# Optimization experiments

Hardware: AMD Instinct MI355X
Metric: run time of the kernel (lower is better)

## Reference

```python
import jax, jax.numpy as jnp
import numpy as np

N = 50000       # nodes
E_RAND = 800000 # random edges (avg degree 16); self loops appended
IN, HID, H, OUT = 256, 64, 4, 256
NEG_SLOPE = 0.2


def setup_inputs() -> dict:
    key = jax.random.key(0)
    ks = jax.random.split(key, 8)
    x = jax.random.normal(ks[0], (N, IN), dtype=jnp.float32)
    er = jax.random.randint(ks[1], (2, E_RAND), 0, N, dtype=jnp.int32)
    loops = jnp.arange(N, dtype=jnp.int32)
    edge_index = jnp.concatenate([er, jnp.stack([loops, loops])], axis=1)  # [2, E_RAND+N]
    # xavier-ish scaled params
    W1 = jax.random.normal(ks[2], (H * HID, IN), jnp.float32) * (2.0 / (IN + H * HID)) ** 0.5
    a1_src = jax.random.normal(ks[3], (H, HID), jnp.float32) * 0.1
    a1_dst = jax.random.normal(ks[4], (H, HID), jnp.float32) * 0.1
    W2 = jax.random.normal(ks[5], (OUT, H * HID), jnp.float32) * (2.0 / (H * HID + OUT)) ** 0.5
    a2_src = jax.random.normal(ks[6], (1, OUT), jnp.float32) * 0.1
    a2_dst = jax.random.normal(ks[7], (1, OUT), jnp.float32) * 0.1
    return {"x": x, "edge_index": edge_index, "W1": W1, "a1_src": a1_src,
            "a1_dst": a1_dst, "W2": W2, "a2_src": a2_src, "a2_dst": a2_dst}


def gat_layer(h, W, a_src, a_dst, src, dst, concat):
    n = h.shape[0]
    nh, nf = a_src.shape
    hp = (h @ W.T).reshape(n, nh, nf)                 # [N,H,F]
    e = (hp[src] * a_src).sum(-1) + (hp[dst] * a_dst).sum(-1)  # [E,H]
    e = jnp.where(e > 0, e, NEG_SLOPE * e)            # leaky_relu
    e_max = jax.ops.segment_max(e, dst, num_segments=n)
    ex = jnp.exp(e - e_max[dst])
    e_sum = jax.ops.segment_sum(ex, dst, num_segments=n)
    alpha = ex / (e_sum[dst] + 1e-16)                 # [E,H]
    out = jax.ops.segment_sum(hp[src] * alpha[..., None], dst, num_segments=n)
    return out.reshape(n, nh * nf) if concat else out.mean(axis=1)


def reference(x, edge_index, W1, a1_src, a1_dst, W2, a2_src, a2_dst):
    src, dst = edge_index[0], edge_index[1]
    h = jax.nn.relu(gat_layer(x, W1, a1_src, a1_dst, src, dst, True))
    return gat_layer(h, W2, a2_src, a2_dst, src, dst, False)
```

## Files before the change

kernel.cpp:

```cpp
#include <hip/hip_runtime.h>
#include <math.h>


typedef __attribute__((ext_vector_type(8))) short short8;
typedef __attribute__((ext_vector_type(4))) float f32x4;
typedef _Float16 half8 __attribute__((ext_vector_type(8)));

__device__ inline short f2bf(float f) {
    unsigned u = __float_as_uint(f);
    unsigned r = (u + 0x7FFF + ((u >> 16) & 1)) >> 16;
    return (short)r;
}
__device__ inline float bf2f(short b) {
    return __uint_as_float(((unsigned)(unsigned short)b) << 16);
}
__device__ inline unsigned short f2h(float f) {
    _Float16 h = (_Float16)f;
    unsigned short u;
    __builtin_memcpy(&u, &h, 2);
    return u;
}
__device__ inline float h2f(unsigned short u) {
    _Float16 h;
    __builtin_memcpy(&h, &u, 2);
    return (float)h;
}

__global__ void convert_w(const float* __restrict__ W, short* __restrict__ Whi,
                          short* __restrict__ Wlo, int n) {
    int i = blockIdx.x * 256 + threadIdx.x;
    if (i < n) {
        float v = W[i];
        short h = f2bf(v);
        Whi[i] = h;
        Wlo[i] = f2bf(v - bf2f(h));
    }
}

__global__ __launch_bounds__(256) void gemm_mfma(const float* __restrict__ A,
                                                 const short* __restrict__ Bh_g,
                                                 const short* __restrict__ Bl_g,
                                                 unsigned short* __restrict__ C, int M) {
    __shared__ short Ah[64 * 40];
    __shared__ short Al[64 * 40];
    __shared__ short Bh[128 * 40];
    __shared__ short Bl[128 * 40];
    const int tid = threadIdx.x;
    const int m0 = blockIdx.x * 64;
    const int n0 = blockIdx.y * 128;
    const int w = tid >> 6, lane = tid & 63;
    const int l15 = lane & 15, q = lane >> 4;

    f32x4 acc[8];
    #pragma unroll
    for (int i = 0; i < 8; ++i) acc[i] = (f32x4){0.f, 0.f, 0.f, 0.f};

    const int ar = tid >> 2;
    const int ak = (tid & 3) * 8;
    const int br = tid >> 1;
    const int bk = (tid & 1) * 16;

    for (int k0 = 0; k0 < 256; k0 += 32) {
        int gm = m0 + ar;
        float4 v0, v1;
        if (gm < M) {
            v0 = *(const float4*)&A[(size_t)gm * 256 + k0 + ak];
            v1 = *(const float4*)&A[(size_t)gm * 256 + k0 + ak + 4];
        } else {
            v0 = make_float4(0.f, 0.f, 0.f, 0.f);
            v1 = v0;
        }
        float av[8] = {v0.x, v0.y, v0.z, v0.w, v1.x, v1.y, v1.z, v1.w};
        short8 hi, lo;
        #pragma unroll
        for (int j = 0; j < 8; ++j) {
            short h = f2bf(av[j]);
            hi[j] = h;
            lo[j] = f2bf(av[j] - bf2f(h));
        }
        *(short8*)&Ah[ar * 40 + ak] = hi;
        *(short8*)&Al[ar * 40 + ak] = lo;
        {
            const short* s0 = &Bh_g[(size_t)(n0 + br) * 256 + k0 + bk];
            *(short8*)&Bh[br * 40 + bk]     = *(const short8*)s0;
            *(short8*)&Bh[br * 40 + bk + 8] = *(const short8*)(s0 + 8);
            const short* s1 = &Bl_g[(size_t)(n0 + br) * 256 + k0 + bk];
            *(short8*)&Bl[br * 40 + bk]     = *(const short8*)s1;
            *(short8*)&Bl[br * 40 + bk + 8] = *(const short8*)(s1 + 8);
        }
        __syncthreads();
        int rowA = w * 16 + l15;
        short8 ahi = *(short8*)&Ah[rowA * 40 + q * 8];
        short8 alo = *(short8*)&Al[rowA * 40 + q * 8];
        #pragma unroll
        for (int nt = 0; nt < 8; ++nt) {
            int rowB = nt * 16 + l15;
            short8 bhi = *(short8*)&Bh[rowB * 40 + q * 8];
            short8 blo = *(short8*)&Bl[rowB * 40 + q * 8];
            acc[nt] = __builtin_amdgcn_mfma_f32_16x16x32_bf16(ahi, bhi, acc[nt], 0, 0, 0);
            acc[nt] = __builtin_amdgcn_mfma_f32_16x16x32_bf16(alo, bhi, acc[nt], 0, 0, 0);
            acc[nt] = __builtin_amdgcn_mfma_f32_16x16x32_bf16(ahi, blo, acc[nt], 0, 0, 0);
        }
        __syncthreads();
    }
    #pragma unroll
    for (int nt = 0; nt < 8; ++nt) {
        #pragma unroll
        for (int r = 0; r < 4; ++r) {
            int gm = m0 + w * 16 + q * 4 + r;
            if (gm < M) C[(size_t)gm * 256 + n0 + nt * 16 + l15] = f2h(acc[nt][r]);
        }
    }
}

__global__ void zero_int(int* __restrict__ p, int n) {
    int i = blockIdx.x * 256 + threadIdx.x;
    if (i < n) p[i] = 0;
}

__global__ void hist_kernel(const int* __restrict__ dst, int* __restrict__ deg, int E) {
    int i = blockIdx.x * 256 + threadIdx.x;
    if (i < E) atomicAdd(&deg[dst[i]], 1);
}

__global__ __launch_bounds__(1024) void scan1(const int* __restrict__ deg,
                                              int* __restrict__ lex,
                                              int* __restrict__ bsums, int n) {
    __shared__ int sh[1024];
    int tid = threadIdx.x;
    int i = blockIdx.x * 1024 + tid;
    int v = (i < n) ? deg[i] : 0;
    sh[tid] = v;
    __syncthreads();
    #pragma unroll
    for (int off = 1; off < 1024; off <<= 1) {
        int t2 = (tid >= off) ? sh[tid - off] : 0;
        __syncthreads();
        sh[tid] += t2;
        __syncthreads();
    }
    if (i < n) lex[i] = sh[tid] - v;
    if (tid == 1023) bsums[blockIdx.x] = sh[1023];
}

__global__ __launch_bounds__(1024) void scan2(const int* __restrict__ bsums,
                                              int* __restrict__ boffs,
                                              int* __restrict__ offs, int nb, int n) {
    __shared__ int sh[1024];
    int tid = threadIdx.x;
    int v = (tid < nb) ? bsums[tid] : 0;
    sh[tid] = v;
    __syncthreads();
    #pragma unroll
    for (int off = 1; off < 1024; off <<= 1) {
        int t2 = (tid >= off) ? sh[tid - off] : 0;
        __syncthreads();
        sh[tid] += t2;
        __syncthreads();
    }
    if (tid < nb) boffs[tid] = sh[tid] - v;
    if (tid == nb - 1) offs[n] = sh[tid];
}

__global__ __launch_bounds__(1024) void scan3(int* __restrict__ offs,
                                              int* __restrict__ cur,
                                              const int* __restrict__ boffs, int n) {
    int i = blockIdx.x * 1024 + threadIdx.x;
    if (i < n) {
        int o = offs[i] + boffs[blockIdx.x];
        offs[i] = o;
        cur[i] = o;
    }
}

__global__ void scatter_kernel(const int* __restrict__ src, const int* __restrict__ dst,
                               int* __restrict__ cur, int* __restrict__ sorted, int E) {
    int i = blockIdx.x * 256 + threadIdx.x;
    if (i < E) {
        int p = atomicAdd(&cur[dst[i]], 1);
        sorted[p] = src[i];
    }
}

template <int NH>
__global__ __launch_bounds__(256) void scompute(const unsigned short* __restrict__ hp,
                                                const float* __restrict__ a_src,
                                                const float* __restrict__ a_dst,
                                                float* __restrict__ s_src,
                                                float* __restrict__ s_dst) {
    __shared__ float w1[4], w2[4];
    int node = blockIdx.x;
    int t = threadIdx.x;
    float v = h2f(hp[(size_t)node * 256 + t]);
    float p1 = v * a_src[t];
    float p2 = v * a_dst[t];
    #pragma unroll
    for (int off = 32; off > 0; off >>= 1) {
        p1 += __shfl_down(p1, off, 64);
        p2 += __shfl_down(p2, off, 64);
    }
    int wave = t >> 6, lane = t & 63;
    if constexpr (NH == 4) {
        if (lane == 0) {
            s_src[node * 4 + wave] = p1;
            s_dst[node * 4 + wave] = p2;
        }
    } else {
        if (lane == 0) { w1[wave] = p1; w2[wave] = p2; }
        __syncthreads();
        if (t == 0) {
            s_src[node] = w1[0] + w1[1] + w1[2] + w1[3];
            s_dst[node] = w2[0] + w2[1] + w2[2] + w2[3];
        }
    }
}

template <int NH, bool RELU>
__global__ __launch_bounds__(256) void aggregate4(const unsigned short* __restrict__ hp,
                                                  const float* __restrict__ ssrc,
                                                  const float* __restrict__ sdst,
                                                  const int* __restrict__ offs,
                                                  const int* __restrict__ sorted,
                                                  float* __restrict__ out, int N) {
    __shared__ int   s_sh[4][64];
    __shared__ float p_sh[4][64][NH];

    const int w = threadIdx.x >> 6, lane = threadIdx.x & 63;
    const int node_raw = blockIdx.x * 4 + w;
    const bool node_ok = node_raw < N;
    const int node = node_ok ? node_raw : (N - 1);
    constexpr int NF = 256 / NH;

    const int b = offs[node], e = offs[node + 1];
    const int deg = e - b;

    float sv[NH];
    #pragma unroll
    for (int h = 0; h < NH; ++h) sv[h] = sdst[node * NH + h];

    float lv[NH], mx[NH];
    const bool small = (deg <= 64);

    if (small) {
        int key = (lane < deg) ? sorted[b + lane] : 0x7FFFFFFF;
        #pragma unroll
        for (int k = 2; k <= 64; k <<= 1) {
            #pragma unroll
            for (int j = k >> 1; j > 0; j >>= 1) {
                int other = __shfl_xor(key, j, 64);
                bool keepMin = ((lane & j) == 0) == ((lane & k) == 0);
                int mn = min(key, other), mh = max(key, other);
                key = keepMin ? mn : mh;
            }
        }
        const bool valid = lane < deg;
        const int mys = valid ? key : 0;

        float evv[NH];
        if constexpr (NH == 4) {
            float4 sa = *(const float4*)&ssrc[(size_t)mys * 4];
            evv[0] = sa.x + sv[0]; evv[1] = sa.y + sv[1];
            evv[2] = sa.z + sv[2]; evv[3] = sa.w + sv[3];
        } else {
            evv[0] = ssrc[mys] + sv[0];
        }
        #pragma unroll
        for (int h = 0; h < NH; ++h) {
            float ev = evv[h];
            ev = ev > 0.f ? ev : 0.2f * ev;
            evv[h] = valid ? ev : -INFINITY;
            mx[h] = evv[h];
        }
        #pragma unroll
        for (int off = 32; off > 0; off >>= 1)
            #pragma unroll
            for (int h = 0; h < NH; ++h)
                mx[h] = fmaxf(mx[h], __shfl_xor(mx[h], off, 64));

        float pv[NH];
        #pragma unroll
        for (int h = 0; h < NH; ++h) {
            pv[h] = valid ? __expf(evv[h] - mx[h]) : 0.f;
            lv[h] = pv[h];
        }
        #pragma unroll
        for (int off = 32; off > 0; off >>= 1)
            #pragma unroll
            for (int h = 0; h < NH; ++h)
                lv[h] += __shfl_xor(lv[h], off, 64);

        s_sh[w][lane] = mys;
        #pragma unroll
        for (int h = 0; h < NH; ++h) p_sh[w][lane][h] = pv[h];
    } else {
        #pragma unroll
        for (int h = 0; h < NH; ++h) mx[h] = -INFINITY;
        for (int c = b + lane; c < e; c += 64) {
            int s = sorted[c];
            #pragma unroll
            for (int h = 0; h < NH; ++h) {
                float ev = ssrc[s * NH + h] + sv[h];
                ev = ev > 0.f ? ev : 0.2f * ev;
                mx[h] = fmaxf(mx[h], ev);
            }
        }
        #pragma unroll
        for (int off = 32; off > 0; off >>= 1)
            #pragma unroll
            for (int h = 0; h < NH; ++h)
                mx[h] = fmaxf(mx[h], __shfl_xor(mx[h], off, 64));
    }

    __syncthreads();

    if (small) {
        const int quarter = lane >> 4;
        const int l16 = lane & 15;
        const int f0 = l16 * 16;
        const int head = f0 / NF;

        float acc[16];
        #pragma unroll
        for (int k = 0; k < 16; ++k) acc[k] = 0.f;

        const int iters = (deg + 3) >> 2;
        for (int t2 = 0; t2 < iters; ++t2) {
            int j = 4 * t2 + quarter;
            bool jv = j < deg;
            int jj = jv ? j : 0;
            int s = s_sh[w][jj];
            float p = jv ? p_sh[w][jj][head] : 0.f;
            const unsigned short* row = hp + (size_t)s * 256 + f0;
            half8 v0 = *(const half8*)(row);
            half8 v1 = *(const half8*)(row + 8);
            #pragma unroll
            for (int k = 0; k < 8; ++k) {
                acc[k]     = fmaf(p, (float)v0[k], acc[k]);
                acc[8 + k] = fmaf(p, (float)v1[k], acc[8 + k]);
            }
        }
        #pragma unroll
        for (int k = 0; k < 16; ++k) {
            acc[k] += __shfl_xor(acc[k], 16, 64);
            acc[k] += __shfl_xor(acc[k], 32, 64);
        }
        if (node_ok && lane < 16) {
            float li = 1.0f / (lv[head] + 1e-16f);
            float o[16];
            #pragma unroll
            for (int k = 0; k < 16; ++k) {
                o[k] = acc[k] * li;
                if (RELU) o[k] = fmaxf(o[k], 0.f);
            }
            float* op = &out[(size_t)node * 256 + f0];
            *(float4*)&op[0]  = make_float4(o[0], o[1], o[2], o[3]);
            *(float4*)&op[4]  = make_float4(o[4], o[5], o[6], o[7]);
            *(float4*)&op[8]  = make_float4(o[8], o[9], o[10], o[11]);
            *(float4*)&op[12] = make_float4(o[12], o[13], o[14], o[15]);
        }
    } else {
        const int half = lane >> 5;
        const int l32 = lane & 31;
        const int f0 = l32 * 8;
        const int head = f0 / NF;

        float acc[8];
        #pragma unroll
        for (int k = 0; k < 8; ++k) acc[k] = 0.f;
        #pragma unroll
        for (int h = 0; h < NH; ++h) lv[h] = 0.f;

        int last = -1, round = 0;
        for (;;) {
            int myMin = 0x7FFFFFFF, myCnt = 0;
            for (int c = b + lane; c < e; c += 64) {
                int s = sorted[c];
                if (s > last) {
                    if (s < myMin) { myMin = s; myCnt = 1; }
                    else if (s == myMin) ++myCnt;
                }
            }
            #pragma unroll
            for (int off = 32; off > 0; off >>= 1) {
                int om = __shfl_xor(myMin, off, 64);
                int oc = __shfl_xor(myCnt, off, 64);
                if (om < myMin) { myMin = om; myCnt = oc; }
                else if (om == myMin) myCnt += oc;
            }
            if (myMin == 0x7FFFFFFF) break;
            const bool mine = ((round & 1) == half);
            float cf = (float)myCnt;
            float ph[NH];
            #pragma unroll
            for (int h = 0; h < NH; ++h) {
                float ev = ssrc[myMin * NH + h] + sv[h];
                ev = ev > 0.f ? ev : 0.2f * ev;
                ph[h] = __expf(ev - mx[h]);
            }
            if (mine && l32 == 0) {
                #pragma unroll
                for (int h = 0; h < NH; ++h) lv[h] += cf * ph[h];
            }
            if (mine) {
                float p = cf * ph[head];
                half8 v = *(const half8*)(hp + (size_t)myMin * 256 + f0);
                #pragma unroll
                for (int k = 0; k < 8; ++k) acc[k] = fmaf(p, (float)v[k], acc[k]);
            }
            last = myMin; ++round;
        }
        #pragma unroll
        for (int off = 32; off > 0; off >>= 1)
            #pragma unroll
            for (int h = 0; h < NH; ++h)
                lv[h] += __shfl_xor(lv[h], off, 64);

        #pragma unroll
        for (int k = 0; k < 8; ++k) acc[k] += __shfl_xor(acc[k], 32, 64);

        if (node_ok && lane < 32) {
            float li = 1.0f / (lv[head] + 1e-16f);
            float o[8];
            #pragma unroll
            for (int k = 0; k < 8; ++k) {
                o[k] = acc[k] * li;
                if (RELU) o[k] = fmaxf(o[k], 0.f);
            }
            *(float4*)&out[(size_t)node * 256 + f0]     = make_float4(o[0], o[1], o[2], o[3]);
            *(float4*)&out[(size_t)node * 256 + f0 + 4] = make_float4(o[4], o[5], o[6], o[7]);
        }
    }
}

extern "C" void kernel_launch(void* const* d_in, const int* in_sizes, int n_in,
                              void* d_out, int out_size, void* d_ws, size_t ws_size,
                              hipStream_t stream) {
    const float* x   = (const float*)d_in[0];
    const int*   ei  = (const int*)d_in[1];
    const float* W1  = (const float*)d_in[2];
    const float* a1s = (const float*)d_in[3];
    const float* a1d = (const float*)d_in[4];
    const float* W2  = (const float*)d_in[5];
    const float* a2s = (const float*)d_in[6];
    const float* a2d = (const float*)d_in[7];
    float* out = (float*)d_out;

    const int N = in_sizes[0] / 256;
    const int E = in_sizes[1] / 2;
    const int* src = ei;
    const int* dst = ei + E;

    unsigned short* hp = (unsigned short*)d_ws;
    float* ssrc  = (float*)(hp + (size_t)N * 256);
    float* sdst  = ssrc + (size_t)N * 4;
    int*   deg   = (int*)(sdst + (size_t)N * 4);
    int*   cur   = deg + N;
    int*   offs  = cur + N;
    int*   sorted= offs + N + 1;
    int*   bsums = sorted + E;
    int*   boffs = bsums + 64;
    short* w1hi  = (short*)(boffs + 64);
    short* w1lo  = w1hi + 65536;
    short* w2hi  = w1lo + 65536;
    short* w2lo  = w2hi + 65536;

    const int nb = (N + 1023) / 1024;

    convert_w<<<256, 256, 0, stream>>>(W1, w1hi, w1lo, 65536);
    convert_w<<<256, 256, 0, stream>>>(W2, w2hi, w2lo, 65536);

    zero_int<<<(N + 255) / 256, 256, 0, stream>>>(deg, N);
    hist_kernel<<<(E + 255) / 256, 256, 0, stream>>>(dst, deg, E);
    scan1<<<nb, 1024, 0, stream>>>(deg, offs, bsums, N);
    scan2<<<1, 1024, 0, stream>>>(bsums, boffs, offs, nb, N);
    scan3<<<nb, 1024, 0, stream>>>(offs, cur, boffs, N);
    scatter_kernel<<<(E + 255) / 256, 256, 0, stream>>>(src, dst, cur, sorted, E);

    dim3 gg((N + 63) / 64, 2);
    int aggblocks = (N + 3) / 4;

    gemm_mfma<<<gg, 256, 0, stream>>>(x, w1hi, w1lo, hp, N);
    scompute<4><<<N, 256, 0, stream>>>(hp, a1s, a1d, ssrc, sdst);
    aggregate4<4, true><<<aggblocks, 256, 0, stream>>>(hp, ssrc, sdst, offs, sorted, out, N);

    gemm_mfma<<<gg, 256, 0, stream>>>(out, w2hi, w2lo, hp, N);
    scompute<1><<<N, 256, 0, stream>>>(hp, a2s, a2d, ssrc, sdst);
    aggregate4<1, false><<<aggblocks, 256, 0, stream>>>(hp, ssrc, sdst, offs, sorted, out, N);
}
```

Baseline: 461.3 us.

## Enlarge GEMM M-tile to 128 and compute attention scores one node per wave

The MFMA GEMM block now covers 128 rows instead of 64, with each wave computing two 16-row subtiles. This lets every B fragment loaded from shared memory feed twice as many MFMAs and halves the number of blocks that reload W. The score kernel now maps one node to a wave with vectorized 4-element loads and xor-shuffle reductions, replacing one 256-thread block per node and removing its shared-memory sync. The trade-offs are more accumulator registers and LDS per GEMM block, which may lower occupancy, and fewer GEMM blocks (about 782 in total) to spread across the GPU.

```diff
diff --git a/kernel.cpp b/kernel.cpp
--- a/kernel.cpp
+++ b/kernel.cpp
@@ -41,74 +41,96 @@
                                                  const short* __restrict__ Bh_g,
                                                  const short* __restrict__ Bl_g,
                                                  unsigned short* __restrict__ C, int M) {
-    __shared__ short Ah[64 * 40];
-    __shared__ short Al[64 * 40];
+    __shared__ short Ah[128 * 40];
+    __shared__ short Al[128 * 40];
     __shared__ short Bh[128 * 40];
     __shared__ short Bl[128 * 40];
     const int tid = threadIdx.x;
-    const int m0 = blockIdx.x * 64;
+    const int m0 = blockIdx.x * 128;
     const int n0 = blockIdx.y * 128;
     const int w = tid >> 6, lane = tid & 63;
     const int l15 = lane & 15, q = lane >> 4;
 
-    f32x4 acc[8];
+    f32x4 acc[2][8];
     #pragma unroll
-    for (int i = 0; i < 8; ++i) acc[i] = (f32x4){0.f, 0.f, 0.f, 0.f};
-
-    const int ar = tid >> 2;
-    const int ak = (tid & 3) * 8;
-    const int br = tid >> 1;
-    const int bk = (tid & 1) * 16;
+    for (int mt = 0; mt < 2; ++mt)
+        #pragma unroll
+        for (int nt = 0; nt < 8; ++nt) acc[mt][nt] = (f32x4){0.f, 0.f, 0.f, 0.f};
+
+    const int ar = tid >> 1;
+    const int ak = (tid & 1) * 16;
 
     for (int k0 = 0; k0 < 256; k0 += 32) {
         int gm = m0 + ar;
-        float4 v0, v1;
+        float4 v0, v1, v2, v3;
         if (gm < M) {
-            v0 = *(const float4*)&A[(size_t)gm * 256 + k0 + ak];
-            v1 = *(const float4*)&A[(size_t)gm * 256 + k0 + ak + 4];
+            const float* ap = &A[(size_t)gm * 256 + k0 + ak];
+            v0 = *(const float4*)(ap);
+            v1 = *(const float4*)(ap + 4);
+            v2 = *(const float4*)(ap + 8);
+            v3 = *(const float4*)(ap + 12);
         } else {
             v0 = make_float4(0.f, 0.f, 0.f, 0.f);
-            v1 = v0;
-        }
-        float av[8] = {v0.x, v0.y, v0.z, v0.w, v1.x, v1.y, v1.z, v1.w};
-        short8 hi, lo;
+            v1 = v0; v2 = v0; v3 = v0;
+        }
+        float av[16] = {v0.x, v0.y, v0.z, v0.w, v1.x, v1.y, v1.z, v1.w,
+                        v2.x, v2.y, v2.z, v2.w, v3.x, v3.y, v3.z, v3.w};
+        short8 hi0, hi1, lo0, lo1;
         #pragma unroll
         for (int j = 0; j < 8; ++j) {
             short h = f2bf(av[j]);
-            hi[j] = h;
-            lo[j] = f2bf(av[j] - bf2f(h));
-        }
-        *(short8*)&Ah[ar * 40 + ak] = hi;
-        *(short8*)&Al[ar * 40 + ak] = lo;
+            hi0[j] = h;
+            lo0[j] = f2bf(av[j] - bf2f(h));
+        }
+        #pragma unroll
+        for (int j = 0; j < 8; ++j) {
+            short h = f2bf(av[8 + j]);
+            hi1[j] = h;
+            lo1[j] = f2bf(av[8 + j] - bf2f(h));
+        }
+        *(short8*)&Ah[ar * 40 + ak]     = hi0;
+        *(short8*)&Ah[ar * 40 + ak + 8] = hi1;
+        *(short8*)&Al[ar * 40 + ak]     = lo0;
+        *(short8*)&Al[ar * 40 + ak + 8] = lo1;
         {
-            const short* s0 = &Bh_g[(size_t)(n0 + br) * 256 + k0 + bk];
-            *(short8*)&Bh[br * 40 + bk]     = *(const short8*)s0;
-            *(short8*)&Bh[br * 40 + bk + 8] = *(const short8*)(s0 + 8);
-            const short* s1 = &Bl_g[(size_t)(n0 + br) * 256 + k0 + bk];
-            *(short8*)&Bl[br * 40 + bk]     = *(const short8*)s1;
-            *(short8*)&Bl[br * 40 + bk + 8] = *(const short8*)(s1 + 8);
+            const short* s0 = &Bh_g[(size_t)(n0 + ar) * 256 + k0 + ak];
+            *(short8*)&Bh[ar * 40 + ak]     = *(const short8*)s0;
+            *(short8*)&Bh[ar * 40 + ak + 8] = *(const short8*)(s0 + 8);
+            const short* s1 = &Bl_g[(size_t)(n0 + ar) * 256 + k0 + ak];
+            *(short8*)&Bl[ar * 40 + ak]     = *(const short8*)s1;
+            *(short8*)&Bl[ar * 40 + ak + 8] = *(const short8*)(s1 + 8);
         }
         __syncthreads();
-        int rowA = w * 16 + l15;
-        short8 ahi = *(short8*)&Ah[rowA * 40 + q * 8];
-        short8 alo = *(short8*)&Al[rowA * 40 + q * 8];
+        short8 ahi[2], alo[2];
+        #pragma unroll
+        for (int mt = 0; mt < 2; ++mt) {
+            int rowA = w * 32 + mt * 16 + l15;
+            ahi[mt] = *(short8*)&Ah[rowA * 40 + q * 8];
+            alo[mt] = *(short8*)&Al[rowA * 40 + q * 8];
+        }
         #pragma unroll
         for (int nt = 0; nt < 8; ++nt) {
             int rowB = nt * 16 + l15;
             short8 bhi = *(short8*)&Bh[rowB * 40 + q * 8];
             short8 blo = *(short8*)&Bl[rowB * 40 + q * 8];
-            acc[nt] = __builtin_amdgcn_mfma_f32_16x16x32_bf16(ahi, bhi, acc[nt], 0, 0, 0);
-            acc[nt] = __builtin_amdgcn_mfma_f32_16x16x32_bf16(alo, bhi, acc[nt], 0, 0, 0);
-            acc[nt] = __builtin_amdgcn_mfma_f32_16x16x32_bf16(ahi, blo, acc[nt], 0, 0, 0);
+            #pragma unroll
+            for (int mt = 0; mt < 2; ++mt) {
+                acc[mt][nt] = __builtin_amdgcn_mfma_f32_16x16x32_bf16(ahi[mt], bhi, acc[mt][nt], 0, 0, 0);
+                acc[mt][nt] = __builtin_amdgcn_mfma_f32_16x16x32_bf16(alo[mt], bhi, acc[mt][nt], 0, 0, 0);
+                acc[mt][nt] = __builtin_amdgcn_mfma_f32_16x16x32_bf16(ahi[mt], blo, acc[mt][nt], 0, 0, 0);
+            }
         }
         __syncthreads();
     }
     #pragma unroll
-    for (int nt = 0; nt < 8; ++nt) {
-        #pragma unroll
-        for (int r = 0; r < 4; ++r) {
-            int gm = m0 + w * 16 + q * 4 + r;
-            if (gm < M) C[(size_t)gm * 256 + n0 + nt * 16 + l15] = f2h(acc[nt][r]);
+    for (int mt = 0; mt < 2; ++mt) {
+        #pragma unroll
+        for (int nt = 0; nt < 8; ++nt) {
+            #pragma unroll
+            for (int r = 0; r < 4; ++r) {
+                int gm = m0 + w * 32 + mt * 16 + q * 4 + r;
+                if (gm < M) C[(size_t)gm * 256 + n0 + nt * 16 + l15] = f2h(acc[mt][nt][r]);
+            }
         }
     }
 }
@@ -187,30 +209,36 @@
                                                 const float* __restrict__ a_src,
                                                 const float* __restrict__ a_dst,
                                                 float* __restrict__ s_src,
-                                                float* __restrict__ s_dst) {
-    __shared__ float w1[4], w2[4];
-    int node = blockIdx.x;
-    int t = threadIdx.x;
-    float v = h2f(hp[(size_t)node * 256 + t]);
-    float p1 = v * a_src[t];
-    float p2 = v * a_dst[t];
-    #pragma unroll
-    for (int off = 32; off > 0; off >>= 1) {
-        p1 += __shfl_down(p1, off, 64);
-        p2 += __shfl_down(p2, off, 64);
-    }
-    int wave = t >> 6, lane = t & 63;
+                                                float* __restrict__ s_dst, int N) {
+    const int w = threadIdx.x >> 6, lane = threadIdx.x & 63;
+    const int node = blockIdx.x * 4 + w;
+    if (node >= N) return;
+    const int f0 = lane * 4;
+    ushort4 uv = *(const ushort4*)(hp + (size_t)node * 256 + f0);
+    float4 as = *(const float4*)(a_src + f0);
+    float4 ad = *(const float4*)(a_dst + f0);
+    float x0 = h2f(uv.x), x1 = h2f(uv.y), x2 = h2f(uv.z), x3 = h2f(uv.w);
+    float p1 = x0 * as.x + x1 * as.y + x2 * as.z + x3 * as.w;
+    float p2 = x0 * ad.x + x1 * ad.y + x2 * ad.z + x3 * ad.w;
     if constexpr (NH == 4) {
+        #pragma unroll
+        for (int off = 1; off < 16; off <<= 1) {
+            p1 += __shfl_xor(p1, off, 64);
+            p2 += __shfl_xor(p2, off, 64);
+        }
+        if ((lane & 15) == 0) {
+            s_src[node * 4 + (lane >> 4)] = p1;
+            s_dst[node * 4 + (lane >> 4)] = p2;
+        }
+    } else {
+        #pragma unroll
+        for (int off = 1; off < 64; off <<= 1) {
+            p1 += __shfl_xor(p1, off, 64);
+            p2 += __shfl_xor(p2, off, 64);
+        }
         if (lane == 0) {
-            s_src[node * 4 + wave] = p1;
-            s_dst[node * 4 + wave] = p2;
-        }
-    } else {
-        if (lane == 0) { w1[wave] = p1; w2[wave] = p2; }
-        __syncthreads();
-        if (t == 0) {
-            s_src[node] = w1[0] + w1[1] + w1[2] + w1[3];
-            s_dst[node] = w2[0] + w2[1] + w2[2] + w2[3];
+            s_src[node] = p1;
+            s_dst[node] = p2;
         }
     }
 }
@@ -476,14 +504,14 @@
     scan3<<<nb, 1024, 0, stream>>>(offs, cur, boffs, N);
     scatter_kernel<<<(E + 255) / 256, 256, 0, stream>>>(src, dst, cur, sorted, E);
 
-    dim3 gg((N + 63) / 64, 2);
+    dim3 gg((N + 127) / 128, 2);
     int aggblocks = (N + 3) / 4;
 
     gemm_mfma<<<gg, 256, 0, stream>>>(x, w1hi, w1lo, hp, N);
-    scompute<4><<<N, 256, 0, stream>>>(hp, a1s, a1d, ssrc, sdst);
+    scompute<4><<<aggblocks, 256, 0, stream>>>(hp, a1s, a1d, ssrc, sdst, N);
     aggregate4<4, true><<<aggblocks, 256, 0, stream>>>(hp, ssrc, sdst, offs, sorted, out, N);
 
     gemm_mfma<<<gg, 256, 0, stream>>>(out, w2hi, w2lo, hp, N);
-    scompute<1><<<N, 256, 0, stream>>>(hp, a2s, a2d, ssrc, sdst);
+    scompute<1><<<aggblocks, 256, 0, stream>>>(hp, a2s, a2d, ssrc, sdst, N);
     aggregate4<1, false><<<aggblocks, 256, 0, stream>>>(hp, ssrc, sdst, offs, sorted, out, N);
 }
```

New measurement: 428.1 us. -7.2%, faster.
